# Kernel tuning notes

Measured on AMD Instinct MI355X. Metric: run time of the kernel, lower is better.

The kernel has to match this reference:

```python
import jax, jax.numpy as jnp
import numpy as np

N_NODES = 50000
N_EDGES = 640000
IN_CH = 128
HID_CH = 256


def setup_inputs() -> dict:
    key = jax.random.key(0)
    k_x, k_e, k_wl, k_bl, k_wr = jax.random.split(key, 5)
    x = jax.random.normal(k_x, (N_NODES, IN_CH), dtype=jnp.float32)
    edge_index = jax.random.randint(k_e, (2, N_EDGES), 0, N_NODES, dtype=jnp.int64)
    # PyG SAGEConv params: lin_l (applied to aggregated neighbors, with bias),
    # lin_r (root/self weight, no bias). Glorot-ish init scale.
    s = 1.0 / np.sqrt(IN_CH)
    W_l = jax.random.uniform(k_wl, (IN_CH, HID_CH), jnp.float32, -s, s)
    b_l = jnp.zeros((HID_CH,), dtype=jnp.float32)
    W_r = jax.random.uniform(k_wr, (IN_CH, HID_CH), jnp.float32, -s, s)
    return {"x": x, "edge_index": edge_index, "W_l": W_l, "b_l": b_l, "W_r": W_r}


def reference(x, edge_index, W_l, b_l, W_r):
    src, dst = edge_index[0], edge_index[1]
    # Gather source-node features per edge and mean-aggregate onto targets.
    msgs = x[src]                                            # [E, in]
    agg = jax.ops.segment_sum(msgs, dst, num_segments=N_NODES)   # [N, in]
    cnt = jax.ops.segment_sum(jnp.ones((N_EDGES,), x.dtype), dst,
                              num_segments=N_NODES)          # [N]
    mean = agg / jnp.maximum(cnt, 1.0)[:, None]
    # out = lin_l(mean_neighbors) + lin_r(x)
    return mean @ W_l + b_l + x @ W_r
```

## Files before the change

### kernel.cpp

```cpp
#include <hip/hip_runtime.h>


constexpr int N_NODES = 50000;
constexpr int N_EDGES = 640000;
constexpr int GEMM_TILES = (N_NODES + 63) / 64;
constexpr int CAP = 64;

constexpr int SCAT_BLOCKS  = N_EDGES / 1024;
constexpr int PREPX_BLOCKS = N_NODES * 32 / 256;
constexpr int WPREP_BLOCKS = 256;

typedef __attribute__((ext_vector_type(8))) short short8;
typedef __attribute__((ext_vector_type(4))) float f32x4;
typedef _Float16 half8 __attribute__((ext_vector_type(8)));

__device__ inline unsigned short f2h(float f) {
    _Float16 h = (_Float16)f;
    return __builtin_bit_cast(unsigned short, h);
}

__global__ __launch_bounds__(256) void prep_k(const float* __restrict__ x,
                                              const int* __restrict__ ei,
                                              const float* __restrict__ Wl,
                                              const float* __restrict__ Wr,
                                              unsigned int* __restrict__ Abf_u,
                                              unsigned short* __restrict__ Wimg,
                                              int* __restrict__ cnt,
                                              int* __restrict__ slots) {
    int bid = blockIdx.x, tid = threadIdx.x;
    if (bid < SCAT_BLOCKS) {
        int base = bid * 1024 + tid;
#pragma unroll
        for (int k = 0; k < 4; k++) {
            int e   = base + k * 256;
            int src = ei[e];
            int dst = ei[N_EDGES + e];
            int pos = atomicAdd(&cnt[dst], 1);
            if (pos < CAP) slots[dst * CAP + pos] = src;
        }
    } else if (bid < SCAT_BLOCKS + PREPX_BLOCKS) {
        int t = (bid - SCAT_BLOCKS) * 256 + tid;
        float4 v = reinterpret_cast<const float4*>(x)[t];
        unsigned int p0 = (unsigned int)f2h(v.x) | ((unsigned int)f2h(v.y) << 16);
        unsigned int p1 = (unsigned int)f2h(v.z) | ((unsigned int)f2h(v.w) << 16);
        int row = t >> 5, c = t & 31;
        reinterpret_cast<uint2*>(Abf_u)[(size_t)row * 64 + 32 + c] =
            make_uint2(p0, p1);
    } else {
        int t = (bid - SCAT_BLOCKS - PREPX_BLOCKS) * 256 + tid;
        int k = t >> 8, n = t & 255;
        float v = (k < 128) ? Wl[k * 256 + n] : Wr[(k - 128) * 256 + n];
        Wimg[(size_t)(k >> 5) * 8192 + n * 32 + (k & 31)] = f2h(v);
    }
}

__global__ __launch_bounds__(256) void agg_k(const int* __restrict__ cnt,
                                             const int* __restrict__ slots,
                                             unsigned int* __restrict__ Abf_u) {
    int wave = (blockIdx.x * 256 + threadIdx.x) >> 6;
    int lane = threadIdx.x & 63;
    int g    = lane >> 4;
    int sub  = lane & 15;
    int node = wave * 4 + g;
    int deg  = cnt[node];
    if (deg > CAP) deg = CAP;
    const int* sl = slots + (size_t)node * CAP;
    const half8* X8 = reinterpret_cast<const half8*>(Abf_u);

    half8 acc = {0, 0, 0, 0, 0, 0, 0, 0};

#define LOADV(vj, J)                                                    \
    half8 vj = {0, 0, 0, 0, 0, 0, 0, 0};                                \
    if (base + (J) < deg)                                               \
        vj = X8[(size_t)sl[base + (J)] * 32 + 16 + sub];

    for (int base = 0; base < deg; base += 16) {
        {
            LOADV(v0, 0) LOADV(v1, 1) LOADV(v2, 2) LOADV(v3, 3)
            LOADV(v4, 4) LOADV(v5, 5) LOADV(v6, 6) LOADV(v7, 7)
            acc += ((v0 + v1) + (v2 + v3)) + ((v4 + v5) + (v6 + v7));
        }
        {
            LOADV(v0, 8)  LOADV(v1, 9)  LOADV(v2, 10) LOADV(v3, 11)
            LOADV(v4, 12) LOADV(v5, 13) LOADV(v6, 14) LOADV(v7, 15)
            acc += ((v0 + v1) + (v2 + v3)) + ((v4 + v5) + (v6 + v7));
        }
    }
#undef LOADV

    int dc = cnt[node];
    float inv = (dc > 0) ? 1.0f / (float)dc : 0.0f;
    half8 o;
#pragma unroll
    for (int j = 0; j < 8; j++) o[j] = (_Float16)((float)acc[j] * inv);
    reinterpret_cast<half8*>(Abf_u)[(size_t)node * 32 + sub] = o;
}

__global__ __launch_bounds__(256) void gemm_k(const unsigned short* __restrict__ Abf,
                                              const unsigned short* __restrict__ Wimg,
                                              const float* __restrict__ bl,
                                              float* __restrict__ out) {
    __shared__ unsigned short As[64 * 40];
    __shared__ unsigned short Bs[256 * 40];

    int tid  = threadIdx.x;
    int w    = tid >> 6;
    int lane = tid & 63;
    int m15  = lane & 15;
    int quad = lane >> 4;
    int bm   = blockIdx.x * 64;

    f32x4 zero4 = {0.f, 0.f, 0.f, 0.f};
    f32x4 acc[4][4];
#pragma unroll
    for (int rt = 0; rt < 4; rt++)
#pragma unroll
        for (int ct = 0; ct < 4; ct++) acc[rt][ct] = zero4;

    for (int kc = 0; kc < 8; kc++) {
        {
            int row = tid >> 2, q = tid & 3;
            int grow = bm + row;
            short8 v = {0, 0, 0, 0, 0, 0, 0, 0};
            if (grow < N_NODES)
                v = *reinterpret_cast<const short8*>(
                        Abf + (size_t)grow * 256 + kc * 32 + q * 8);
            *reinterpret_cast<short8*>(As + row * 40 + q * 8) = v;
        }
        {
            const unsigned short* src = Wimg + (size_t)kc * 8192 + tid * 32;
#pragma unroll
            for (int s = 0; s < 4; s++) {
                short8 v = *reinterpret_cast<const short8*>(src + s * 8);
                *reinterpret_cast<short8*>(Bs + tid * 40 + s * 8) = v;
            }
        }
        __syncthreads();

        half8 Af[4], Bf[4];
#pragma unroll
        for (int rt = 0; rt < 4; rt++)
            Af[rt] = *reinterpret_cast<const half8*>(
                         As + (rt * 16 + m15) * 40 + quad * 8);
#pragma unroll
        for (int ct = 0; ct < 4; ct++)
            Bf[ct] = *reinterpret_cast<const half8*>(
                         Bs + (w * 64 + ct * 16 + m15) * 40 + quad * 8);
#pragma unroll
        for (int rt = 0; rt < 4; rt++)
#pragma unroll
            for (int ct = 0; ct < 4; ct++)
                acc[rt][ct] = __builtin_amdgcn_mfma_f32_16x16x32_f16(
                    Af[rt], Bf[ct], acc[rt][ct], 0, 0, 0);
        __syncthreads();
    }

    float bias[4];
#pragma unroll
    for (int ct = 0; ct < 4; ct++) bias[ct] = bl[w * 64 + ct * 16 + m15];
#pragma unroll
    for (int rt = 0; rt < 4; rt++) {
        int rb = bm + rt * 16 + quad * 4;
#pragma unroll
        for (int r = 0; r < 4; r++) {
            int row = rb + r;
            if (row < N_NODES) {
#pragma unroll
                for (int ct = 0; ct < 4; ct++)
                    out[(size_t)row * 256 + w * 64 + ct * 16 + m15] =
                        acc[rt][ct][r] + bias[ct];
            }
        }
    }
}

extern "C" void kernel_launch(void* const* d_in, const int* in_sizes, int n_in,
                              void* d_out, int out_size, void* d_ws, size_t ws_size,
                              hipStream_t stream) {
    const float* x  = (const float*)d_in[0];
    const int*   ei = (const int*)d_in[1];
    const float* Wl = (const float*)d_in[2];
    const float* bl = (const float*)d_in[3];
    const float* Wr = (const float*)d_in[4];
    float* out = (float*)d_out;

    unsigned short* Abf  = (unsigned short*)d_ws;
    unsigned short* Wimg = Abf + (size_t)N_NODES * 256;
    int* cnt   = (int*)(Wimg + 65536);
    int* slots = cnt + N_NODES;

    hipMemsetAsync(cnt, 0, N_NODES * sizeof(int), stream);

    prep_k<<<SCAT_BLOCKS + PREPX_BLOCKS + WPREP_BLOCKS, 256, 0, stream>>>(
        x, ei, Wl, Wr, (unsigned int*)Abf, Wimg, cnt, slots);
    agg_k<<<(N_NODES / 4 * 64) / 256, 256, 0, stream>>>(cnt, slots,
                                                        (unsigned int*)Abf);
    gemm_k<<<GEMM_TILES, 256, 0, stream>>>(Abf, Wimg, bl, out);
}
```

Before: 173.8 us.

## Enlarge GEMM tile to 128 rows with 512 threads and shuffle-broadcast slot indices

The GEMM block now covers 128 output rows using 8 waves arranged 2x4, so each weight chunk staged in shared memory is reused across twice as many rows and global weight traffic is halved. In the aggregation kernel, each lane loads one neighbor index per 16-edge chunk and the indices are broadcast with __shfl instead of every lane loading every index, and the degree read is reused. Larger blocks cut the grid count and may reduce occupancy or worsen tail balance.

```diff
diff --git a/kernel.cpp b/kernel.cpp
--- a/kernel.cpp
+++ b/kernel.cpp
@@ -3,7 +3,7 @@
 
 constexpr int N_NODES = 50000;
 constexpr int N_EDGES = 640000;
-constexpr int GEMM_TILES = (N_NODES + 63) / 64;
+constexpr int GEMM_TILES = (N_NODES + 127) / 128;
 constexpr int CAP = 64;
 
 constexpr int SCAT_BLOCKS  = N_EDGES / 1024;
@@ -36,7 +36,7 @@
             int src = ei[e];
             int dst = ei[N_EDGES + e];
             int pos = atomicAdd(&cnt[dst], 1);
-            if (pos < CAP) slots[dst * CAP + pos] = src;
+            if (pos < CAP) slots[(size_t)dst * CAP + pos] = src;
         }
     } else if (bid < SCAT_BLOCKS + PREPX_BLOCKS) {
         int t = (bid - SCAT_BLOCKS) * 256 + tid;
@@ -62,8 +62,8 @@
     int g    = lane >> 4;
     int sub  = lane & 15;
     int node = wave * 4 + g;
-    int deg  = cnt[node];
-    if (deg > CAP) deg = CAP;
+    int dc   = cnt[node];
+    int deg  = (dc > CAP) ? CAP : dc;
     const int* sl = slots + (size_t)node * CAP;
     const half8* X8 = reinterpret_cast<const half8*>(Abf_u);
 
@@ -71,10 +71,14 @@
 
 #define LOADV(vj, J)                                                    \
     half8 vj = {0, 0, 0, 0, 0, 0, 0, 0};                                \
-    if (base + (J) < deg)                                               \
-        vj = X8[(size_t)sl[base + (J)] * 32 + 16 + sub];
+    {                                                                   \
+        int sj = __shfl(slv, (J), 16);                                  \
+        if (base + (J) < deg)                                           \
+            vj = X8[(size_t)sj * 32 + 16 + sub];                        \
+    }
 
     for (int base = 0; base < deg; base += 16) {
+        int slv = sl[base + sub];
         {
             LOADV(v0, 0) LOADV(v1, 1) LOADV(v2, 2) LOADV(v3, 3)
             LOADV(v4, 4) LOADV(v5, 5) LOADV(v6, 6) LOADV(v7, 7)
@@ -88,7 +92,6 @@
     }
 #undef LOADV
 
-    int dc = cnt[node];
     float inv = (dc > 0) ? 1.0f / (float)dc : 0.0f;
     half8 o;
 #pragma unroll
@@ -96,19 +99,21 @@
     reinterpret_cast<half8*>(Abf_u)[(size_t)node * 32 + sub] = o;
 }
 
-__global__ __launch_bounds__(256) void gemm_k(const unsigned short* __restrict__ Abf,
+__global__ __launch_bounds__(512) void gemm_k(const unsigned short* __restrict__ Abf,
                                               const unsigned short* __restrict__ Wimg,
                                               const float* __restrict__ bl,
                                               float* __restrict__ out) {
-    __shared__ unsigned short As[64 * 40];
+    __shared__ unsigned short As[128 * 40];
     __shared__ unsigned short Bs[256 * 40];
 
     int tid  = threadIdx.x;
-    int w    = tid >> 6;
+    int w8   = tid >> 6;
+    int wm   = w8 >> 2;
+    int wn   = w8 & 3;
     int lane = tid & 63;
     int m15  = lane & 15;
     int quad = lane >> 4;
-    int bm   = blockIdx.x * 64;
+    int bm   = blockIdx.x * 128;
 
     f32x4 zero4 = {0.f, 0.f, 0.f, 0.f};
     f32x4 acc[4][4];
@@ -128,11 +133,14 @@
             *reinterpret_cast<short8*>(As + row * 40 + q * 8) = v;
         }
         {
-            const unsigned short* src = Wimg + (size_t)kc * 8192 + tid * 32;
-#pragma unroll
-            for (int s = 0; s < 4; s++) {
+            int n = tid >> 1, half = tid & 1;
+            const unsigned short* src =
+                Wimg + (size_t)kc * 8192 + n * 32 + half * 16;
+            unsigned short* dstp = Bs + n * 40 + half * 16;
+#pragma unroll
+            for (int s = 0; s < 2; s++) {
                 short8 v = *reinterpret_cast<const short8*>(src + s * 8);
-                *reinterpret_cast<short8*>(Bs + tid * 40 + s * 8) = v;
+                *reinterpret_cast<short8*>(dstp + s * 8) = v;
             }
         }
         __syncthreads();
@@ -141,11 +149,11 @@
 #pragma unroll
         for (int rt = 0; rt < 4; rt++)
             Af[rt] = *reinterpret_cast<const half8*>(
-                         As + (rt * 16 + m15) * 40 + quad * 8);
+                         As + (wm * 64 + rt * 16 + m15) * 40 + quad * 8);
 #pragma unroll
         for (int ct = 0; ct < 4; ct++)
             Bf[ct] = *reinterpret_cast<const half8*>(
-                         Bs + (w * 64 + ct * 16 + m15) * 40 + quad * 8);
+                         Bs + (wn * 64 + ct * 16 + m15) * 40 + quad * 8);
 #pragma unroll
         for (int rt = 0; rt < 4; rt++)
 #pragma unroll
@@ -157,17 +165,17 @@
 
     float bias[4];
 #pragma unroll
-    for (int ct = 0; ct < 4; ct++) bias[ct] = bl[w * 64 + ct * 16 + m15];
+    for (int ct = 0; ct < 4; ct++) bias[ct] = bl[wn * 64 + ct * 16 + m15];
 #pragma unroll
     for (int rt = 0; rt < 4; rt++) {
-        int rb = bm + rt * 16 + quad * 4;
+        int rb = bm + wm * 64 + rt * 16 + quad * 4;
 #pragma unroll
         for (int r = 0; r < 4; r++) {
             int row = rb + r;
             if (row < N_NODES) {
 #pragma unroll
                 for (int ct = 0; ct < 4; ct++)
-                    out[(size_t)row * 256 + w * 64 + ct * 16 + m15] =
+                    out[(size_t)row * 256 + wn * 64 + ct * 16 + m15] =
                         acc[rt][ct][r] + bias[ct];
             }
         }
@@ -195,5 +203,5 @@
         x, ei, Wl, Wr, (unsigned int*)Abf, Wimg, cnt, slots);
     agg_k<<<(N_NODES / 4 * 64) / 256, 256, 0, stream>>>(cnt, slots,
                                                         (unsigned int*)Abf);
-    gemm_k<<<GEMM_TILES, 256, 0, stream>>>(Abf, Wimg, bl, out);
-}
+    gemm_k<<<GEMM_TILES, 512, 0, stream>>>(Abf, Wimg, bl, out);
+}
```

Measured after the change: 162.7 us. 6.4% less time.
